# Kernel optimization log

Measured on AMD Instinct MI355X. Metric: run time of the kernel, lower is better.

The kernel has to match this reference:

```python
import jax, jax.numpy as jnp
import numpy as np

BSZ, DIM, SEQ_A, SEQ_B = 16, 768, 1024, 1024


def setup_inputs() -> dict:
    key = jax.random.key(0)
    kA, kB, kU = jax.random.split(key, 3)
    input_A = jax.random.normal(kA, (BSZ, DIM, SEQ_A), dtype=jnp.float32)
    input_B = jax.random.normal(kB, (BSZ, DIM, SEQ_B), dtype=jnp.float32)
    intput_msk = jnp.zeros((BSZ, SEQ_A, SEQ_B), dtype=jnp.float32)  # 0 = on, -inf = off
    U = jax.random.normal(kU, (DIM, DIM), dtype=jnp.float32)
    return {"input_A": input_A, "input_B": input_B, "intput_msk": intput_msk, "U": U}


def reference(input_A, input_B, intput_msk, U):
    # align[b,s,t] = tanh( A[b,:,s]^T U B[b,:,t] )  -> (bsz, seq_A, seq_B)
    align = jnp.einsum("bds,de,bet->bst", input_A, U, input_B)
    align = jnp.tanh(align) + intput_msk
    # per-token scores: max over the other modality's sequence, then softmax
    score_A = jax.nn.softmax(jnp.max(align, axis=2), axis=-1)  # (bsz, seq_A)
    score_B = jax.nn.softmax(jnp.max(align, axis=1), axis=-1)  # (bsz, seq_B)
    output_A = jnp.einsum("bds,bs->bd", input_A, score_A)  # (bsz, dim_A)
    output_B = jnp.einsum("bdt,bt->bd", input_B, score_B)  # (bsz, dim_B)
    return (output_A, output_B)
```

## Files before the change

### kernel.cpp

```cpp
#include <hip/hip_runtime.h>
#include <math.h>

#define BSZ  16
#define DIM  768
#define SEQA 1024
#define SEQB 1024

typedef float f32x4 __attribute__((ext_vector_type(4)));
typedef long long llong;

__device__ inline void gload_lds16(const void* g, void* l) {
    __builtin_amdgcn_global_load_lds(
        (const __attribute__((address_space(1))) void*)g,
        (__attribute__((address_space(3))) void*)l, 16, 0, 0);
}

__device__ inline unsigned enc_key(float f) {
    unsigned u = __float_as_uint(f);
    return (u & 0x80000000u) ? ~u : (u | 0x80000000u);
}
__device__ inline float dec_key(unsigned k) {
    return (k & 0x80000000u) ? __uint_as_float(k ^ 0x80000000u) : __uint_as_float(~k);
}

__device__ inline unsigned pk4_fp8(float a, float b, float c, float d) {
    int v = 0;
    v = __builtin_amdgcn_cvt_pk_fp8_f32(a, b, v, false);
    v = __builtin_amdgcn_cvt_pk_fp8_f32(c, d, v, true);
    return (unsigned)v;
}
__device__ inline unsigned char f2fp8(float a) {
    return (unsigned char)(__builtin_amdgcn_cvt_pk_fp8_f32(a, a, 0, false) & 0xFF);
}
__device__ inline unsigned short f2bf(float f) {
    unsigned u = __float_as_uint(f);
    return (unsigned short)((u + 0x7FFF + ((u >> 16) & 1)) >> 16);
}
__device__ inline float bf2f(unsigned short h) {
    return __uint_as_float((unsigned)h << 16);
}

__device__ inline float fast_tanh(float x) {
    float ax = fabsf(x);
    float u = __expf(-2.0f * ax);
    float th = __fdividef(1.0f - u, 1.0f + u);
    return copysignf(th, x);
}

__global__ __launch_bounds__(256) void t_cast_AB(const float* __restrict__ A,
                                                 const float* __restrict__ B,
                                                 unsigned char* __restrict__ At,
                                                 unsigned char* __restrict__ Bt,
                                                 unsigned short* __restrict__ At16,
                                                 unsigned short* __restrict__ Bt16,
                                                 int w16) {
    __shared__ float tl[64][68];
    const int z = blockIdx.z;
    const float* X = (z < BSZ) ? A : B;
    unsigned char* Y = (z < BSZ) ? At : Bt;
    unsigned short* Y16 = (z < BSZ) ? At16 : Bt16;
    const int b = z & 15;
    const int d0 = blockIdx.y * 64;
    const int s0 = blockIdx.x * 64;
    const int tid = threadIdx.x;
    const int rr = tid >> 4, c4 = tid & 15;
    const float* Xb = X + ((size_t)b * DIM + d0) * SEQA + s0;
#pragma unroll
    for (int i = 0; i < 4; i++) {
        int row = i * 16 + rr;
        float4 v = *(const float4*)&Xb[(size_t)row * SEQA + c4 * 4];
        *(float4*)&tl[row][c4 * 4] = v;
    }
    __syncthreads();
    const int m = tid & 15, sl = tid >> 4;
    unsigned char* Yb = Y + ((size_t)b * SEQA + s0) * DIM + d0;
#pragma unroll
    for (int i = 0; i < 4; i++) {
        int s = sl + 16 * i;
        unsigned v = pk4_fp8(tl[4 * m + 0][s], tl[4 * m + 1][s], tl[4 * m + 2][s], tl[4 * m + 3][s]);
        *(unsigned*)&Yb[(size_t)s * DIM + 4 * m] = v;
    }
    if (w16) {
        unsigned short* Yc = Y16 + ((size_t)b * SEQA + s0) * DIM + d0;
#pragma unroll
        for (int i = 0; i < 4; i++) {
            int s = sl + 16 * i;
            uint2 w;
            w.x = (unsigned)f2bf(tl[4 * m + 0][s]) | ((unsigned)f2bf(tl[4 * m + 1][s]) << 16);
            w.y = (unsigned)f2bf(tl[4 * m + 2][s]) | ((unsigned)f2bf(tl[4 * m + 3][s]) << 16);
            *(uint2*)&Yc[(size_t)s * DIM + 4 * m] = w;
        }
    }
}

__global__ __launch_bounds__(256) void t_cast_U(const float* __restrict__ U,
                                                unsigned char* __restrict__ Ut,
                                                unsigned* __restrict__ keyA,
                                                unsigned* __restrict__ keyB) {
    __shared__ float tl[64][68];
    const int d0 = blockIdx.y * 64;
    const int e0 = blockIdx.x * 64;
    const int tid = threadIdx.x;
    const int bid = blockIdx.y * gridDim.x + blockIdx.x;
    if (bid < 64) {
        int i = bid * 256 + tid;
        keyA[i] = 0u;
        keyB[i] = 0u;
    }
    const int rr = tid >> 4, c4 = tid & 15;
#pragma unroll
    for (int i = 0; i < 4; i++) {
        int row = i * 16 + rr;
        float4 v = *(const float4*)&U[(size_t)(d0 + row) * DIM + e0 + c4 * 4];
        *(float4*)&tl[row][c4 * 4] = v;
    }
    __syncthreads();
    const int m = tid & 15, sl = tid >> 4;
#pragma unroll
    for (int i = 0; i < 4; i++) {
        int e = sl + 16 * i;
        unsigned v = pk4_fp8(tl[4 * m + 0][e], tl[4 * m + 1][e], tl[4 * m + 2][e], tl[4 * m + 3][e]);
        *(unsigned*)&Ut[(size_t)(e0 + e) * DIM + d0 + 4 * m] = v;
    }
}

__device__ inline void stage_tile(const unsigned char* __restrict__ src, int row0,
                                  int kbyte0, unsigned char* lds, int wid, int lane) {
    const int r8 = lane >> 3;
    const int g  = lane & 7;
    const int gg = g ^ (r8 & 7);
#pragma unroll
    for (int t = 0; t < 4; ++t) {
        int row = row0 + wid * 32 + t * 8 + r8;
        gload_lds16(src + (size_t)row * DIM + kbyte0 + gg * 16,
                    lds + (wid * 32 + t * 8) * 128 + lane * 16);
    }
}

__device__ inline llong frag_read(const unsigned char* lds, int rowbase, int l15,
                                  int quad, int h) {
    int gg = 2 * h + (quad >> 1);
    int off = (rowbase + l15) * 128 + ((gg ^ (l15 & 7)) << 4) + (quad & 1) * 8;
    return *(const llong*)(lds + off);
}

__global__ __launch_bounds__(256) void k1_ua(const unsigned char* __restrict__ At,
                                             const unsigned char* __restrict__ Ut,
                                             unsigned char* __restrict__ Ct) {
    __shared__ __align__(16) unsigned char As[128 * 128];
    __shared__ __align__(16) unsigned char Us[128 * 128];
    const int b  = blockIdx.z;
    const int s0 = blockIdx.x * 128;
    const int e0 = blockIdx.y * 128;
    const int tid = threadIdx.x;
    const int lane = tid & 63;
    const int wid = tid >> 6;
    const int wr = wid >> 1, wc = wid & 1;
    const int quad = lane >> 4, l15 = lane & 15;

    const unsigned char* Atb = At + (size_t)b * SEQA * DIM;
    f32x4 acc[4][4] = {};

    for (int d0 = 0; d0 < DIM; d0 += 128) {
        stage_tile(Atb + (size_t)s0 * DIM, 0, d0, As, wid, lane);
        stage_tile(Ut + (size_t)e0 * DIM, 0, d0, Us, wid, lane);
        __syncthreads();
#pragma unroll
        for (int h = 0; h < 4; ++h) {
            llong av[4], bv[4];
#pragma unroll
            for (int i = 0; i < 4; ++i) av[i] = frag_read(As, wr * 64 + 16 * i, l15, quad, h);
#pragma unroll
            for (int j = 0; j < 4; ++j) bv[j] = frag_read(Us, wc * 64 + 16 * j, l15, quad, h);
#pragma unroll
            for (int i = 0; i < 4; ++i)
#pragma unroll
                for (int j = 0; j < 4; ++j)
                    acc[i][j] = __builtin_amdgcn_mfma_f32_16x16x32_fp8_fp8(av[i], bv[j], acc[i][j], 0, 0, 0);
        }
        __syncthreads();
    }
    unsigned char* Cb = Ct + (size_t)b * SEQA * DIM;
#pragma unroll
    for (int i = 0; i < 4; ++i)
#pragma unroll
        for (int j = 0; j < 4; ++j) {
            int e_g = e0 + wc * 64 + 16 * j + l15;
#pragma unroll
            for (int r = 0; r < 4; ++r) {
                int s_g = s0 + wr * 64 + 16 * i + quad * 4 + r;
                Cb[(size_t)s_g * DIM + e_g] = f2fp8(acc[i][j][r]);
            }
        }
}

__global__ __launch_bounds__(256, 2) void k2_align(const unsigned char* __restrict__ Ct,
                                                   const unsigned char* __restrict__ Bt,
                                                   const float* __restrict__ msk,
                                                   unsigned* __restrict__ keyA,
                                                   unsigned* __restrict__ keyB) {
    __shared__ __align__(16) unsigned char Cs[128 * 128];
    __shared__ __align__(16) unsigned char Bs[128 * 128];
    const int b  = blockIdx.z;
    const int t0 = blockIdx.x * 128;
    const int s0 = blockIdx.y * 128;
    const int tid = threadIdx.x;
    const int lane = tid & 63;
    const int wid = tid >> 6;
    const int wr = wid >> 1, wc = wid & 1;
    const int quad = lane >> 4, l15 = lane & 15;

    const float* Mb = msk + (size_t)b * SEQA * SEQB;
    float4 mv[4][4];
#pragma unroll
    for (int i = 0; i < 4; ++i)
#pragma unroll
        for (int j = 0; j < 4; ++j) {
            int s_g = s0 + wc * 64 + 16 * j + l15;
            int t_g = t0 + wr * 64 + 16 * i + quad * 4;
            mv[i][j] = *(const float4*)&Mb[(size_t)s_g * SEQB + t_g];
        }

    f32x4 acc[4][4] = {};

    for (int e0 = 0; e0 < DIM; e0 += 128) {
        stage_tile(Ct + (size_t)(b * SEQA + s0) * DIM, 0, e0, Cs, wid, lane);
        stage_tile(Bt + (size_t)(b * SEQB + t0) * DIM, 0, e0, Bs, wid, lane);
        __syncthreads();
#pragma unroll
        for (int h = 0; h < 4; ++h) {
            llong av[4], bv[4];
#pragma unroll
            for (int i = 0; i < 4; ++i) av[i] = frag_read(Bs, wr * 64 + 16 * i, l15, quad, h);
#pragma unroll
            for (int j = 0; j < 4; ++j) bv[j] = frag_read(Cs, wc * 64 + 16 * j, l15, quad, h);
#pragma unroll
            for (int i = 0; i < 4; ++i)
#pragma unroll
                for (int j = 0; j < 4; ++j)
                    acc[i][j] = __builtin_amdgcn_mfma_f32_16x16x32_fp8_fp8(av[i], bv[j], acc[i][j], 0, 0, 0);
        }
        __syncthreads();
    }

#pragma unroll
    for (int i = 0; i < 4; ++i)
#pragma unroll
        for (int j = 0; j < 4; ++j) {
            acc[i][j][0] = fast_tanh(acc[i][j][0]) + mv[i][j].x;
            acc[i][j][1] = fast_tanh(acc[i][j][1]) + mv[i][j].y;
            acc[i][j][2] = fast_tanh(acc[i][j][2]) + mv[i][j].z;
            acc[i][j][3] = fast_tanh(acc[i][j][3]) + mv[i][j].w;
        }
#pragma unroll
    for (int j = 0; j < 4; ++j) {
        float m = -INFINITY;
#pragma unroll
        for (int i = 0; i < 4; ++i)
#pragma unroll
            for (int r = 0; r < 4; ++r) m = fmaxf(m, acc[i][j][r]);
        m = fmaxf(m, __shfl_xor(m, 16));
        m = fmaxf(m, __shfl_xor(m, 32));
        if (quad == 0)
            atomicMax(&keyA[b * SEQA + s0 + wc * 64 + 16 * j + l15], enc_key(m));
    }
#pragma unroll
    for (int i = 0; i < 4; ++i)
#pragma unroll
        for (int r = 0; r < 4; ++r) {
            float m = fmaxf(fmaxf(acc[i][0][r], acc[i][1][r]), fmaxf(acc[i][2][r], acc[i][3][r]));
            m = fmaxf(m, __shfl_xor(m, 1));
            m = fmaxf(m, __shfl_xor(m, 2));
            m = fmaxf(m, __shfl_xor(m, 4));
            m = fmaxf(m, __shfl_xor(m, 8));
            if (l15 == 0)
                atomicMax(&keyB[b * SEQB + t0 + wr * 64 + 16 * i + quad * 4 + r], enc_key(m));
        }
}

__global__ __launch_bounds__(256) void k3_softmax(const unsigned* __restrict__ keyA,
                                                  const unsigned* __restrict__ keyB,
                                                  float* __restrict__ scoreA,
                                                  float* __restrict__ scoreB) {
    const int b = blockIdx.x;
    const bool isA = (blockIdx.y == 0);
    const unsigned* keys = isA ? (keyA + b * SEQA) : (keyB + b * SEQB);
    float* score = isA ? (scoreA + b * SEQA) : (scoreB + b * SEQB);
    __shared__ float sh[4];
    const int tid = threadIdx.x;
    float m[4];
    float mx = -INFINITY;
#pragma unroll
    for (int k = 0; k < 4; k++) {
        m[k] = dec_key(keys[tid + 256 * k]);
        mx = fmaxf(mx, m[k]);
    }
#pragma unroll
    for (int o = 32; o > 0; o >>= 1) mx = fmaxf(mx, __shfl_down(mx, o, 64));
    if ((tid & 63) == 0) sh[tid >> 6] = mx;
    __syncthreads();
    mx = fmaxf(fmaxf(sh[0], sh[1]), fmaxf(sh[2], sh[3]));
    __syncthreads();
    float e[4];
    float sum = 0.f;
#pragma unroll
    for (int k = 0; k < 4; k++) { e[k] = expf(m[k] - mx); sum += e[k]; }
#pragma unroll
    for (int o = 32; o > 0; o >>= 1) sum += __shfl_down(sum, o, 64);
    if ((tid & 63) == 0) sh[tid >> 6] = sum;
    __syncthreads();
    sum = sh[0] + sh[1] + sh[2] + sh[3];
    float inv = 1.0f / sum;
#pragma unroll
    for (int k = 0; k < 4; k++) score[tid + 256 * k] = e[k] * inv;
}

__global__ __launch_bounds__(256) void k4_bf16(const unsigned short* __restrict__ At16,
                                               const unsigned short* __restrict__ Bt16,
                                               const float* __restrict__ scoreA,
                                               const float* __restrict__ scoreB,
                                               float* __restrict__ out) {
    const int sc = blockIdx.x;
    const int which = blockIdx.y;
    const int b = blockIdx.z;
    const unsigned short* X = which ? Bt16 : At16;
    const float* S = which ? scoreB : scoreA;
    __shared__ float sh[128];
    const int tid = threadIdx.x;
    if (tid < 128) sh[tid] = S[b * SEQA + sc * 128 + tid];
    __syncthreads();
    const unsigned short* Xb = X + ((size_t)b * SEQA + sc * 128) * DIM;
    float a0 = 0.f, a1 = 0.f, a2 = 0.f;
    for (int s = 0; s < 128; ++s) {
        float f = sh[s];
        const unsigned short* row = Xb + (size_t)s * DIM;
        a0 += f * bf2f(row[tid]);
        a1 += f * bf2f(row[tid + 256]);
        a2 += f * bf2f(row[tid + 512]);
    }
    float* o = out + which * (BSZ * DIM) + b * DIM;
    atomicAdd(&o[tid], a0);
    atomicAdd(&o[tid + 256], a1);
    atomicAdd(&o[tid + 512], a2);
}

__global__ __launch_bounds__(256) void k4_f32(const float* __restrict__ A,
                                              const float* __restrict__ B,
                                              const float* __restrict__ scoreA,
                                              const float* __restrict__ scoreB,
                                              float* __restrict__ out) {
    const int which = blockIdx.y;
    const int row = blockIdx.x * 4 + (threadIdx.x >> 6);
    const int lane = threadIdx.x & 63;
    const float* X = which ? B : A;
    const float* S = which ? scoreB : scoreA;
    const int b = row / DIM;
    const float4* xr = (const float4*)(X + (size_t)row * SEQA);
    const float4* sr = (const float4*)(S + (size_t)b * SEQA);
    float acc = 0.f;
#pragma unroll
    for (int q = lane; q < SEQA / 4; q += 64) {
        float4 x = xr[q];
        float4 s = sr[q];
        acc += x.x * s.x + x.y * s.y + x.z * s.z + x.w * s.w;
    }
#pragma unroll
    for (int o = 32; o > 0; o >>= 1) acc += __shfl_down(acc, o, 64);
    if (lane == 0) out[which * (BSZ * DIM) + row] = acc;
}

extern "C" void kernel_launch(void* const* d_in, const int* in_sizes, int n_in,
                              void* d_out, int out_size, void* d_ws, size_t ws_size,
                              hipStream_t stream) {
    const float* A   = (const float*)d_in[0];
    const float* B   = (const float*)d_in[1];
    const float* msk = (const float*)d_in[2];
    const float* U   = (const float*)d_in[3];
    float* out = (float*)d_out;

    char* ws = (char*)d_ws;
    unsigned char* At = (unsigned char*)ws;
    unsigned char* Bt = (unsigned char*)(ws + 12582912);
    unsigned char* Ct = (unsigned char*)(ws + 25165824);
    unsigned char* Ut = (unsigned char*)(ws + 37748736);
    unsigned* keyA   = (unsigned*)(ws + 38338560);
    unsigned* keyB   = (unsigned*)(ws + 38404096);
    float*    scoreA = (float*)   (ws + 38469632);
    float*    scoreB = (float*)   (ws + 38535168);
    unsigned short* At16 = (unsigned short*)(ws + 38600704);
    unsigned short* Bt16 = (unsigned short*)(ws + 63766528);
    const int w16 = (ws_size >= 88932352ull) ? 1 : 0;

    t_cast_U<<<dim3(DIM / 64, DIM / 64, 1), 256, 0, stream>>>(U, Ut, keyA, keyB);
    t_cast_AB<<<dim3(SEQA / 64, DIM / 64, 2 * BSZ), 256, 0, stream>>>(A, B, At, Bt, At16, Bt16, w16);
    k1_ua<<<dim3(SEQA / 128, DIM / 128, BSZ), 256, 0, stream>>>(At, Ut, Ct);
    k2_align<<<dim3(SEQB / 128, SEQA / 128, BSZ), 256, 0, stream>>>(Ct, Bt, msk, keyA, keyB);
    k3_softmax<<<dim3(BSZ, 2), 256, 0, stream>>>(keyA, keyB, scoreA, scoreB);
    if (w16) {
        hipMemsetAsync(d_out, 0, (size_t)out_size * sizeof(float), stream);
        k4_bf16<<<dim3(8, 2, BSZ), 256, 0, stream>>>(At16, Bt16, scoreA, scoreB, out);
    } else {
        k4_f32<<<dim3(BSZ * DIM / 4, 2), 256, 0, stream>>>(A, B, scoreA, scoreB, out);
    }
}
```

Before: 252.1 us.

## Enlarge GEMM block tiles, fuse output zeroing into softmax, vectorize k4 loads

The U·A GEMM now computes 256x128 tiles with 512 threads, and the alignment GEMM computes 256x256 tiles with 1024 threads and 16 waves. Both raise operand reuse from LDS and cut global/L2 traffic for the fp8 operands. The mask load moves after the main loop to lower register pressure during the MFMA loop. The separate memset is replaced by zeroing the output inside the softmax kernel, and the bf16 weighted-sum kernel now reads 4 contiguous bf16 per thread with 192 threads. Larger blocks mean fewer resident blocks per CU and less latency hiding, since there is still no double buffering.

```diff
diff --git a/kernel.cpp b/kernel.cpp
--- a/kernel.cpp
+++ b/kernel.cpp
@@ -124,16 +124,17 @@
     }
 }
 
-__device__ inline void stage_tile(const unsigned char* __restrict__ src, int row0,
-                                  int kbyte0, unsigned char* lds, int wid, int lane) {
+template <int RPW>
+__device__ inline void stage_tileN(const unsigned char* __restrict__ src, int kbyte0,
+                                   unsigned char* lds, int wid, int lane) {
     const int r8 = lane >> 3;
     const int g  = lane & 7;
     const int gg = g ^ (r8 & 7);
 #pragma unroll
-    for (int t = 0; t < 4; ++t) {
-        int row = row0 + wid * 32 + t * 8 + r8;
+    for (int t = 0; t < RPW / 8; ++t) {
+        int row = wid * RPW + t * 8 + r8;
         gload_lds16(src + (size_t)row * DIM + kbyte0 + gg * 16,
-                    lds + (wid * 32 + t * 8) * 128 + lane * 16);
+                    lds + (wid * RPW + t * 8) * 128 + lane * 16);
     }
 }
 
@@ -144,13 +145,13 @@
     return *(const llong*)(lds + off);
 }
 
-__global__ __launch_bounds__(256) void k1_ua(const unsigned char* __restrict__ At,
+__global__ __launch_bounds__(512) void k1_ua(const unsigned char* __restrict__ At,
                                              const unsigned char* __restrict__ Ut,
                                              unsigned char* __restrict__ Ct) {
-    __shared__ __align__(16) unsigned char As[128 * 128];
+    __shared__ __align__(16) unsigned char As[256 * 128];
     __shared__ __align__(16) unsigned char Us[128 * 128];
     const int b  = blockIdx.z;
-    const int s0 = blockIdx.x * 128;
+    const int s0 = blockIdx.x * 256;
     const int e0 = blockIdx.y * 128;
     const int tid = threadIdx.x;
     const int lane = tid & 63;
@@ -158,12 +159,13 @@
     const int wr = wid >> 1, wc = wid & 1;
     const int quad = lane >> 4, l15 = lane & 15;
 
-    const unsigned char* Atb = At + (size_t)b * SEQA * DIM;
+    const unsigned char* Ab = At + (size_t)(b * SEQA + s0) * DIM;
+    const unsigned char* Ub = Ut + (size_t)e0 * DIM;
     f32x4 acc[4][4] = {};
 
     for (int d0 = 0; d0 < DIM; d0 += 128) {
-        stage_tile(Atb + (size_t)s0 * DIM, 0, d0, As, wid, lane);
-        stage_tile(Ut + (size_t)e0 * DIM, 0, d0, Us, wid, lane);
+        stage_tileN<32>(Ab, d0, As, wid, lane);
+        stage_tileN<16>(Ub, d0, Us, wid, lane);
         __syncthreads();
 #pragma unroll
         for (int h = 0; h < 4; ++h) {
@@ -194,63 +196,58 @@
         }
 }
 
-__global__ __launch_bounds__(256, 2) void k2_align(const unsigned char* __restrict__ Ct,
-                                                   const unsigned char* __restrict__ Bt,
-                                                   const float* __restrict__ msk,
-                                                   unsigned* __restrict__ keyA,
-                                                   unsigned* __restrict__ keyB) {
-    __shared__ __align__(16) unsigned char Cs[128 * 128];
-    __shared__ __align__(16) unsigned char Bs[128 * 128];
+__global__ __launch_bounds__(1024) void k2_align(const unsigned char* __restrict__ Ct,
+                                                 const unsigned char* __restrict__ Bt,
+                                                 const float* __restrict__ msk,
+                                                 unsigned* __restrict__ keyA,
+                                                 unsigned* __restrict__ keyB) {
+    __shared__ __align__(16) unsigned char Bs[256 * 128];
+    __shared__ __align__(16) unsigned char Cs[256 * 128];
     const int b  = blockIdx.z;
-    const int t0 = blockIdx.x * 128;
-    const int s0 = blockIdx.y * 128;
+    const int t0 = blockIdx.x * 256;
+    const int s0 = blockIdx.y * 256;
     const int tid = threadIdx.x;
     const int lane = tid & 63;
     const int wid = tid >> 6;
-    const int wr = wid >> 1, wc = wid & 1;
+    const int wr = wid >> 2, wc = wid & 3;
     const int quad = lane >> 4, l15 = lane & 15;
 
+    const unsigned char* Bb = Bt + (size_t)(b * SEQB + t0) * DIM;
+    const unsigned char* Cb = Ct + (size_t)(b * SEQA + s0) * DIM;
+    f32x4 acc[4][4] = {};
+
+    for (int e0 = 0; e0 < DIM; e0 += 128) {
+        stage_tileN<16>(Bb, e0, Bs, wid, lane);
+        stage_tileN<16>(Cb, e0, Cs, wid, lane);
+        __syncthreads();
+#pragma unroll
+        for (int h = 0; h < 4; ++h) {
+            llong av[4], bv[4];
+#pragma unroll
+            for (int i = 0; i < 4; ++i) av[i] = frag_read(Bs, wr * 64 + 16 * i, l15, quad, h);
+#pragma unroll
+            for (int j = 0; j < 4; ++j) bv[j] = frag_read(Cs, wc * 64 + 16 * j, l15, quad, h);
+#pragma unroll
+            for (int i = 0; i < 4; ++i)
+#pragma unroll
+                for (int j = 0; j < 4; ++j)
+                    acc[i][j] = __builtin_amdgcn_mfma_f32_16x16x32_fp8_fp8(av[i], bv[j], acc[i][j], 0, 0, 0);
+        }
+        __syncthreads();
+    }
+
     const float* Mb = msk + (size_t)b * SEQA * SEQB;
-    float4 mv[4][4];
 #pragma unroll
     for (int i = 0; i < 4; ++i)
 #pragma unroll
         for (int j = 0; j < 4; ++j) {
             int s_g = s0 + wc * 64 + 16 * j + l15;
             int t_g = t0 + wr * 64 + 16 * i + quad * 4;
-            mv[i][j] = *(const float4*)&Mb[(size_t)s_g * SEQB + t_g];
-        }
-
-    f32x4 acc[4][4] = {};
-
-    for (int e0 = 0; e0 < DIM; e0 += 128) {
-        stage_tile(Ct + (size_t)(b * SEQA + s0) * DIM, 0, e0, Cs, wid, lane);
-        stage_tile(Bt + (size_t)(b * SEQB + t0) * DIM, 0, e0, Bs, wid, lane);
-        __syncthreads();
-#pragma unroll
-        for (int h = 0; h < 4; ++h) {
-            llong av[4], bv[4];
-#pragma unroll
-            for (int i = 0; i < 4; ++i) av[i] = frag_read(Bs, wr * 64 + 16 * i, l15, quad, h);
-#pragma unroll
-            for (int j = 0; j < 4; ++j) bv[j] = frag_read(Cs, wc * 64 + 16 * j, l15, quad, h);
-#pragma unroll
-            for (int i = 0; i < 4; ++i)
-#pragma unroll
-                for (int j = 0; j < 4; ++j)
-                    acc[i][j] = __builtin_amdgcn_mfma_f32_16x16x32_fp8_fp8(av[i], bv[j], acc[i][j], 0, 0, 0);
-        }
-        __syncthreads();
-    }
-
-#pragma unroll
-    for (int i = 0; i < 4; ++i)
-#pragma unroll
-        for (int j = 0; j < 4; ++j) {
-            acc[i][j][0] = fast_tanh(acc[i][j][0]) + mv[i][j].x;
-            acc[i][j][1] = fast_tanh(acc[i][j][1]) + mv[i][j].y;
-            acc[i][j][2] = fast_tanh(acc[i][j][2]) + mv[i][j].z;
-            acc[i][j][3] = fast_tanh(acc[i][j][3]) + mv[i][j].w;
+            float4 mv = *(const float4*)&Mb[(size_t)s_g * SEQB + t_g];
+            acc[i][j][0] = fast_tanh(acc[i][j][0]) + mv.x;
+            acc[i][j][1] = fast_tanh(acc[i][j][1]) + mv.y;
+            acc[i][j][2] = fast_tanh(acc[i][j][2]) + mv.z;
+            acc[i][j][3] = fast_tanh(acc[i][j][3]) + mv.w;
         }
 #pragma unroll
     for (int j = 0; j < 4; ++j) {
@@ -281,13 +278,20 @@
 __global__ __launch_bounds__(256) void k3_softmax(const unsigned* __restrict__ keyA,
                                                   const unsigned* __restrict__ keyB,
                                                   float* __restrict__ scoreA,
-                                                  float* __restrict__ scoreB) {
+                                                  float* __restrict__ scoreB,
+                                                  float* __restrict__ out) {
     const int b = blockIdx.x;
     const bool isA = (blockIdx.y == 0);
     const unsigned* keys = isA ? (keyA + b * SEQA) : (keyB + b * SEQB);
     float* score = isA ? (scoreA + b * SEQA) : (scoreB + b * SEQB);
+    const int tid = threadIdx.x;
+    {
+        int base = (blockIdx.y * gridDim.x + blockIdx.x) * DIM;
+        out[base + tid] = 0.f;
+        out[base + tid + 256] = 0.f;
+        out[base + tid + 512] = 0.f;
+    }
     __shared__ float sh[4];
-    const int tid = threadIdx.x;
     float m[4];
     float mx = -INFINITY;
 #pragma unroll
@@ -315,7 +319,7 @@
     for (int k = 0; k < 4; k++) score[tid + 256 * k] = e[k] * inv;
 }
 
-__global__ __launch_bounds__(256) void k4_bf16(const unsigned short* __restrict__ At16,
+__global__ __launch_bounds__(192) void k4_bf16(const unsigned short* __restrict__ At16,
                                                const unsigned short* __restrict__ Bt16,
                                                const float* __restrict__ scoreA,
                                                const float* __restrict__ scoreB,
@@ -329,19 +333,22 @@
     const int tid = threadIdx.x;
     if (tid < 128) sh[tid] = S[b * SEQA + sc * 128 + tid];
     __syncthreads();
-    const unsigned short* Xb = X + ((size_t)b * SEQA + sc * 128) * DIM;
-    float a0 = 0.f, a1 = 0.f, a2 = 0.f;
+    const unsigned short* Xb = X + ((size_t)b * SEQA + sc * 128) * DIM + tid * 4;
+    float a0 = 0.f, a1 = 0.f, a2 = 0.f, a3 = 0.f;
+#pragma unroll 4
     for (int s = 0; s < 128; ++s) {
         float f = sh[s];
-        const unsigned short* row = Xb + (size_t)s * DIM;
-        a0 += f * bf2f(row[tid]);
-        a1 += f * bf2f(row[tid + 256]);
-        a2 += f * bf2f(row[tid + 512]);
-    }
-    float* o = out + which * (BSZ * DIM) + b * DIM;
-    atomicAdd(&o[tid], a0);
-    atomicAdd(&o[tid + 256], a1);
-    atomicAdd(&o[tid + 512], a2);
+        uint2 w = *(const uint2*)(Xb + (size_t)s * DIM);
+        a0 += f * bf2f((unsigned short)(w.x & 0xFFFF));
+        a1 += f * bf2f((unsigned short)(w.x >> 16));
+        a2 += f * bf2f((unsigned short)(w.y & 0xFFFF));
+        a3 += f * bf2f((unsigned short)(w.y >> 16));
+    }
+    float* o = out + which * (BSZ * DIM) + b * DIM + tid * 4;
+    atomicAdd(&o[0], a0);
+    atomicAdd(&o[1], a1);
+    atomicAdd(&o[2], a2);
+    atomicAdd(&o[3], a3);
 }
 
 __global__ __launch_bounds__(256) void k4_f32(const float* __restrict__ A,
@@ -393,12 +400,11 @@
 
     t_cast_U<<<dim3(DIM / 64, DIM / 64, 1), 256, 0, stream>>>(U, Ut, keyA, keyB);
     t_cast_AB<<<dim3(SEQA / 64, DIM / 64, 2 * BSZ), 256, 0, stream>>>(A, B, At, Bt, At16, Bt16, w16);
-    k1_ua<<<dim3(SEQA / 128, DIM / 128, BSZ), 256, 0, stream>>>(At, Ut, Ct);
-    k2_align<<<dim3(SEQB / 128, SEQA / 128, BSZ), 256, 0, stream>>>(Ct, Bt, msk, keyA, keyB);
-    k3_softmax<<<dim3(BSZ, 2), 256, 0, stream>>>(keyA, keyB, scoreA, scoreB);
+    k1_ua<<<dim3(SEQA / 256, DIM / 128, BSZ), 512, 0, stream>>>(At, Ut, Ct);
+    k2_align<<<dim3(SEQB / 256, SEQA / 256, BSZ), 1024, 0, stream>>>(Ct, Bt, msk, keyA, keyB);
+    k3_softmax<<<dim3(BSZ, 2), 256, 0, stream>>>(keyA, keyB, scoreA, scoreB, out);
     if (w16) {
-        hipMemsetAsync(d_out, 0, (size_t)out_size * sizeof(float), stream);
-        k4_bf16<<<dim3(8, 2, BSZ), 256, 0, stream>>>(At16, Bt16, scoreA, scoreB, out);
+        k4_bf16<<<dim3(8, 2, BSZ), 192, 0, stream>>>(At16, Bt16, scoreA, scoreB, out);
     } else {
         k4_f32<<<dim3(BSZ * DIM / 4, 2), 256, 0, stream>>>(A, B, scoreA, scoreB, out);
     }
```

Result: slower. 264.3 us (+4.8%).
